# Performance work log

Hardware: AMD Instinct MI355X
Metric: run time of the kernel (lower is better)

## Reference

```python
import jax, jax.numpy as jnp
import numpy as np

N, E, IN_CH, EDGE_DIM, N_GRAPHS = 8000, 64000, 256, 16, 64
HEADS = (3, 2, 2, 1)
OUT_CH = (512, 512, 256, 256)
IN_CHS = (IN_CH, 1536, 1024, 512)
NEG_SLOPE = 0.2  # PyG GATv2Conv default negative_slope


def setup_inputs() -> dict:
    key = jax.random.key(0)
    ks = iter(jax.random.split(key, 64))
    d = {}
    d["x"] = jax.random.normal(next(ks), (N, IN_CH), jnp.float32)
    d["edge_index"] = jax.random.randint(next(ks), (2, E), 0, N, dtype=jnp.int32)
    d["edge_attr"] = jax.random.normal(next(ks), (E, EDGE_DIM), jnp.float32)
    d["batch"] = jnp.sort(jax.random.randint(next(ks), (N,), 0, N_GRAPHS, dtype=jnp.int32))
    for i, (ci, h, co) in enumerate(zip(IN_CHS, HEADS, OUT_CH), 1):
        hc = h * co
        s = 1.0 / np.sqrt(ci)
        d[f"W{i}l"] = (jax.random.normal(next(ks), (ci, hc)) * s).astype(jnp.float32)
        d[f"b{i}l"] = jnp.zeros((hc,), jnp.float32)
        d[f"W{i}r"] = (jax.random.normal(next(ks), (ci, hc)) * s).astype(jnp.float32)
        d[f"b{i}r"] = jnp.zeros((hc,), jnp.float32)
        d[f"W{i}e"] = (jax.random.normal(next(ks), (EDGE_DIM, hc)) / np.sqrt(EDGE_DIM)).astype(jnp.float32)
        d[f"att{i}"] = (jax.random.normal(next(ks), (h, co)) / np.sqrt(co)).astype(jnp.float32)
        d[f"bias{i}"] = jnp.zeros((hc,), jnp.float32)
    d["fc1_w"] = (jax.random.normal(next(ks), (256, 64)) / 16.0).astype(jnp.float32)
    d["fc1_b"] = jnp.zeros((64,), jnp.float32)
    d["fc2_w"] = (jax.random.normal(next(ks), (64, 1)) / 8.0).astype(jnp.float32)
    d["fc2_b"] = jnp.zeros((1,), jnp.float32)
    return d


def gatv2(x, src, dst, ea, Wl, bl, Wr, br, We, att, bias, heads, co):
    """GATv2Conv forward (PyG semantics, self-loops already appended in src/dst/ea)."""
    n = x.shape[0]
    xl = (x @ Wl + bl).reshape(n, heads, co)  # applied to source nodes
    xr = (x @ Wr + br).reshape(n, heads, co)  # applied to target nodes
    ee = (ea @ We).reshape(-1, heads, co)     # edge embedding (no bias in PyG)
    m = xl[src] + xr[dst] + ee                # [E', H, C]
    logits = jnp.einsum('ehc,hc->eh', jax.nn.leaky_relu(m, NEG_SLOPE), att)
    # segmented softmax over incoming edges per destination node
    lmax = jax.ops.segment_max(logits, dst, num_segments=n)
    p = jnp.exp(logits - lmax[dst])
    denom = jax.ops.segment_sum(p, dst, num_segments=n)
    alpha = p / denom[dst]                    # every node has a self-loop -> denom > 0
    out = jax.ops.segment_sum(alpha[:, :, None] * xl[src], dst, num_segments=n)
    return out.reshape(n, heads * co) + bias


def _forward(x, edge_index, edge_attr, batch, params, fc):
    n = x.shape[0]
    src0, dst0 = edge_index[0], edge_index[1]
    # add_self_loops with fill_value='mean': per-destination mean of incoming edge_attr
    ea_sum = jax.ops.segment_sum(edge_attr, dst0, num_segments=n)
    ea_cnt = jax.ops.segment_sum(jnp.ones((edge_attr.shape[0], 1), edge_attr.dtype), dst0, num_segments=n)
    ea_loop = ea_sum / jnp.maximum(ea_cnt, 1.0)
    loop = jnp.arange(n, dtype=edge_index.dtype)
    src = jnp.concatenate([src0, loop])
    dst = jnp.concatenate([dst0, loop])
    ea = jnp.concatenate([edge_attr, ea_loop])
    h = x
    for p, hds, co in zip(params, HEADS, OUT_CH):
        h = jax.nn.relu(gatv2(h, src, dst, ea, *p, hds, co))
    # global mean pool over graphs
    s = jax.ops.segment_sum(h, batch, num_segments=N_GRAPHS)
    cnt = jax.ops.segment_sum(jnp.ones((n, 1), h.dtype), batch, num_segments=N_GRAPHS)
    g = s / jnp.maximum(cnt, 1.0)
    # dropout is identity in eval mode
    fc1_w, fc1_b, fc2_w, fc2_b = fc
    g = jax.nn.relu(g @ fc1_w + fc1_b)
    return g @ fc2_w + fc2_b


def reference(x, edge_index, edge_attr, batch,
              W1l, b1l, W1r, b1r, W1e, att1, bias1,
              W2l, b2l, W2r, b2r, W2e, att2, bias2,
              W3l, b3l, W3r, b3r, W3e, att3, bias3,
              W4l, b4l, W4r, b4r, W4e, att4, bias4,
              fc1_w, fc1_b, fc2_w, fc2_b):
    params = [(W1l, b1l, W1r, b1r, W1e, att1, bias1),
              (W2l, b2l, W2r, b2r, W2e, att2, bias2),
              (W3l, b3l, W3r, b3r, W3e, att3, bias3),
              (W4l, b4l, W4r, b4r, W4e, att4, bias4)]
    return _forward(x, edge_index, edge_attr, batch, params, (fc1_w, fc1_b, fc2_w, fc2_b))
```

## Files before the change

### kernel.cpp

```cpp
#include <hip/hip_runtime.h>
#include <math.h>

#define N_NODES 8000
#define N_EDGES 64000
#define ETOT    (N_EDGES + N_NODES)
#define EDIM    16
#define NGRAPHS 64

typedef __attribute__((ext_vector_type(8))) short short8v;
typedef __attribute__((ext_vector_type(4))) short short4v;
typedef __attribute__((ext_vector_type(4))) float f32x4;

__device__ inline unsigned short f2bf(float f) {
    unsigned u = __builtin_bit_cast(unsigned, f);
    unsigned r = (u + 0x7FFF + ((u >> 16) & 1)) >> 16;
    return (unsigned short)r;
}
__device__ inline float bf2f(unsigned short b) {
    unsigned u = ((unsigned)b) << 16;
    return __builtin_bit_cast(float, u);
}

__device__ inline void gload16(const void* g, void* l) {
    __builtin_amdgcn_global_load_lds(
        (const __attribute__((address_space(1))) void*)g,
        (__attribute__((address_space(3))) void*)l, 16, 0, 0);
}


__global__ void count_deg(const int* __restrict__ dst0, int* __restrict__ deg) {
    int e = blockIdx.x * 256 + threadIdx.x;
    if (e < N_EDGES) atomicAdd(&deg[dst0[e]], 1);
}

__global__ void scan_deg2(const int* __restrict__ deg, int* __restrict__ rowptr,
                          int* __restrict__ woff) {
    __shared__ int stot[256];
    int t = threadIdx.x;
    int base = t * 32;
    int sum = 0;
    for (int j = 0; j < 32; j++) {
        int i = base + j;
        if (i < N_NODES) sum += deg[i] + 1;
    }
    stot[t] = sum;
    __syncthreads();
    for (int off = 1; off < 256; off <<= 1) {
        int u = (t >= off) ? stot[t - off] : 0;
        __syncthreads();
        stot[t] += u;
        __syncthreads();
    }
    int run = (t == 0) ? 0 : stot[t - 1];
    if (t == 0) rowptr[0] = 0;
    for (int j = 0; j < 32; j++) {
        int i = base + j;
        if (i < N_NODES) {
            int v = deg[i] + 1;
            woff[i] = run;
            rowptr[i + 1] = run + v;
            run += v;
        }
    }
}

__global__ void fill_eid(const int* __restrict__ dst0, int* __restrict__ woff,
                         int* __restrict__ eid) {
    int i = blockIdx.x * 256 + threadIdx.x;
    if (i < N_EDGES) {
        int pos = atomicAdd(&woff[dst0[i]], 1);
        eid[pos] = i;
    } else if (i < ETOT) {
        int n = i - N_EDGES;
        int pos = atomicAdd(&woff[n], 1);
        eid[pos] = i;
    }
}

__global__ void csr_fill_dst(const int* __restrict__ rowptr, int* __restrict__ csr_dst) {
    int n = blockIdx.x * 256 + threadIdx.x;
    if (n >= N_NODES) return;
    int b = rowptr[n], t = rowptr[n + 1];
    for (int i = b; i < t; i++) csr_dst[i] = n;
}

__global__ void ea_loop_kernel(const int* __restrict__ rowptr, const int* __restrict__ eid,
                               const float* __restrict__ edge_attr, float* __restrict__ ea_loop) {
    int n = blockIdx.x * 256 + threadIdx.x;
    if (n >= N_NODES) return;
    float s[EDIM];
#pragma unroll
    for (int k = 0; k < EDIM; k++) s[k] = 0.f;
    int cnt = 0;
    int b = rowptr[n], t = rowptr[n + 1];
    for (int i = b; i < t; i++) {
        int e = eid[i];
        if (e < N_EDGES) {
            cnt++;
            const float* ea = edge_attr + (size_t)e * EDIM;
#pragma unroll
            for (int k = 0; k < EDIM; k++) s[k] += ea[k];
        }
    }
    float inv = 1.f / (float)(cnt > 0 ? cnt : 1);
#pragma unroll
    for (int k = 0; k < EDIM; k++) ea_loop[(size_t)n * EDIM + k] = s[k] * inv;
}

__global__ void csr_srcea_bf(const int* __restrict__ eid, const int* __restrict__ src0,
                             const float* __restrict__ edge_attr, const float* __restrict__ ea_loop,
                             int* __restrict__ csr_src,
                             short* __restrict__ eah, short* __restrict__ eal) {
    int t = blockIdx.x * 256 + threadIdx.x;
    int i = t >> 2, q = t & 3;
    if (i >= ETOT) return;
    int e = eid[i];
    int s = (e < N_EDGES) ? src0[e] : (e - N_EDGES);
    if (q == 0) csr_src[i] = s;
    const float* ea = (e < N_EDGES) ? edge_attr + (size_t)e * EDIM
                                    : ea_loop + (size_t)(e - N_EDGES) * EDIM;
    float4 v = *(const float4*)(ea + q * 4);
    unsigned short h0 = f2bf(v.x), h1 = f2bf(v.y), h2 = f2bf(v.z), h3 = f2bf(v.w);
    short4v hv = { (short)h0, (short)h1, (short)h2, (short)h3 };
    short4v lv = { (short)f2bf(v.x - bf2f(h0)), (short)f2bf(v.y - bf2f(h1)),
                   (short)f2bf(v.z - bf2f(h2)), (short)f2bf(v.w - bf2f(h3)) };
    short4v zv = { 0, 0, 0, 0 };
    *(short4v*)(eah + (size_t)i * 32 + q * 4) = hv;
    *(short4v*)(eal + (size_t)i * 32 + q * 4) = lv;
    *(short4v*)(eah + (size_t)i * 32 + 16 + q * 4) = zv;
    *(short4v*)(eal + (size_t)i * 32 + 16 + q * 4) = zv;
}

__global__ void cvt_we_all(const float* __restrict__ We1, const float* __restrict__ We2,
                           const float* __restrict__ We3, const float* __restrict__ We4,
                           short* __restrict__ weTh, short* __restrict__ weTl) {
    int ch = blockIdx.x * 256 + threadIdx.x;
    if (ch >= 3328) return;
    const float* We; int lch, hc;
    if (ch < 1536)      { We = We1; lch = ch;        hc = 1536; }
    else if (ch < 2560) { We = We2; lch = ch - 1536; hc = 1024; }
    else if (ch < 3072) { We = We3; lch = ch - 2560; hc = 512;  }
    else                { We = We4; lch = ch - 3072; hc = 256;  }
#pragma unroll
    for (int k = 0; k < EDIM; k++) {
        float v = We[(size_t)k * hc + lch];
        unsigned short h = f2bf(v);
        unsigned short l = f2bf(v - bf2f(h));
        weTh[(size_t)ch * 32 + k] = (short)h;
        weTl[(size_t)ch * 32 + k] = (short)l;
    }
#pragma unroll
    for (int k = EDIM; k < 32; k++) {
        weTh[(size_t)ch * 32 + k] = 0;
        weTl[(size_t)ch * 32 + k] = 0;
    }
}


__global__ __launch_bounds__(256) void cvt_wt_t2(
        const float* __restrict__ Wl, const float* __restrict__ Wr,
        short* __restrict__ WTh, short* __restrict__ WTl, int K, int Nc) {
    __shared__ float sh[32][33];
    const float* W = blockIdx.z ? Wr : Wl;
    size_t obase = blockIdx.z ? (size_t)Nc * K : 0;
    int t = threadIdx.x;
    int tx = t & 31, ty = t >> 5;
    int n0 = blockIdx.x * 32, k0 = blockIdx.y * 32;
#pragma unroll
    for (int j = 0; j < 4; j++)
        sh[ty + j * 8][tx] = W[(size_t)(k0 + ty + j * 8) * Nc + n0 + tx];
    __syncthreads();
#pragma unroll
    for (int j = 0; j < 4; j++) {
        int row = ty + j * 8;
        float v = sh[tx][row];
        unsigned short h = f2bf(v);
        unsigned short l = f2bf(v - bf2f(h));
        size_t idx = obase + (size_t)(n0 + row) * K + k0 + tx;
        WTh[idx] = (short)h;
        WTl[idx] = (short)l;
    }
}


__global__ __launch_bounds__(256) void cvt_act(
        const float* __restrict__ in, short* __restrict__ acth, short* __restrict__ actl,
        int total ) {
    int i = blockIdx.x * 256 + threadIdx.x;
    if (i * 4 >= total) return;
    float4 v = *(const float4*)(in + (size_t)i * 4);
    unsigned short h0 = f2bf(v.x), h1 = f2bf(v.y), h2 = f2bf(v.z), h3 = f2bf(v.w);
    short4v hv = { (short)h0, (short)h1, (short)h2, (short)h3 };
    short4v lv = { (short)f2bf(v.x - bf2f(h0)), (short)f2bf(v.y - bf2f(h1)),
                   (short)f2bf(v.z - bf2f(h2)), (short)f2bf(v.w - bf2f(h3)) };
    *(short4v*)(acth + (size_t)i * 4) = hv;
    *(short4v*)(actl + (size_t)i * 4) = lv;
}


__global__ __launch_bounds__(256) void gemm_mfma5(
        const short* __restrict__ Ah_g, const short* __restrict__ Al_g,
        const short* __restrict__ BTh, const short* __restrict__ BTl,
        const float* __restrict__ bias1, const float* __restrict__ bias2, int hsplit,
        float* __restrict__ C, int M, int K, int Nc) {
    __shared__ __align__(16) short lds[4 * 128 * 32];
    int t = threadIdx.x;

    int gx = gridDim.x;
    int nwg = gx * gridDim.y;
    int orig = blockIdx.y * gx + blockIdx.x;
    int q = nwg >> 3, r = nwg & 7;
    int xcd = orig & 7, pos = orig >> 3;
    int nid = (xcd < r ? xcd * (q + 1) : r * (q + 1) + (xcd - r) * q) + pos;
    int bx = nid % gx, by = nid / gx;
    int m0 = by * 128, n0 = bx * 128;

    int lane = t & 63, wave = t >> 6;
    int wm = (wave >> 1) * 64, wn = (wave & 1) * 64;
    int fr = lane & 15, quad = lane >> 4;

    int rl = lane >> 2, seg = lane & 3;
    int perm = seg ^ ((rl >> 1) & 3);
    const short* gp = (wave == 0) ? Ah_g : (wave == 1) ? Al_g : (wave == 2) ? BTh : BTl;
    int brow = (wave < 2) ? m0 : n0;
    const short* src = gp + (size_t)(brow + rl) * K + perm * 8;
    short* ldsw = &lds[wave * 4096];

    int ks = (quad ^ ((fr >> 1) & 3)) << 3;

    f32x4 acc[4][4];
#pragma unroll
    for (int i = 0; i < 4; i++)
#pragma unroll
        for (int j = 0; j < 4; j++) acc[i][j] = (f32x4)(0.f);

    for (int k0 = 0; k0 < K; k0 += 32) {
        __syncthreads();
#pragma unroll
        for (int g = 0; g < 8; g++)
            gload16(src + k0 + (size_t)g * 16 * K, ldsw + g * 512);
        __syncthreads();

        short8v ah[4], al[4], bh[4], bl[4];
#pragma unroll
        for (int mi = 0; mi < 4; mi++) {
            int rr = (wm + mi * 16 + fr) * 32 + ks;
            ah[mi] = *(short8v*)&lds[rr];
            al[mi] = *(short8v*)&lds[4096 + rr];
        }
#pragma unroll
        for (int ni = 0; ni < 4; ni++) {
            int rr = (wn + ni * 16 + fr) * 32 + ks;
            bh[ni] = *(short8v*)&lds[8192 + rr];
            bl[ni] = *(short8v*)&lds[12288 + rr];
        }
#pragma unroll
        for (int mi = 0; mi < 4; mi++)
#pragma unroll
            for (int ni = 0; ni < 4; ni++) {
                acc[mi][ni] = __builtin_amdgcn_mfma_f32_16x16x32_bf16(
                    al[mi], bh[ni], acc[mi][ni], 0, 0, 0);
                acc[mi][ni] = __builtin_amdgcn_mfma_f32_16x16x32_bf16(
                    ah[mi], bl[ni], acc[mi][ni], 0, 0, 0);
                acc[mi][ni] = __builtin_amdgcn_mfma_f32_16x16x32_bf16(
                    ah[mi], bh[ni], acc[mi][ni], 0, 0, 0);
            }
    }

    int rbase = (lane >> 4) * 4;
#pragma unroll
    for (int ni = 0; ni < 4; ni++) {
        int col = n0 + wn + ni * 16 + fr;
        const float* bp = (col < hsplit) ? bias1 + col : bias2 + (col - hsplit);
        float bz = *bp;
#pragma unroll
        for (int mi = 0; mi < 4; mi++) {
            int row0 = m0 + wm + mi * 16 + rbase;
#pragma unroll
            for (int rr = 0; rr < 4; rr++) {
                int row = row0 + rr;
                if (row < M) C[(size_t)row * Nc + col] = acc[mi][ni][rr] + bz;
            }
        }
    }
}


__global__ __launch_bounds__(256, 4) void edge_logits7(
        const float* __restrict__ xl, const float* __restrict__ xr,
        const short* __restrict__ weTh, const short* __restrict__ weTl,
        const float* __restrict__ att,
        const short* __restrict__ eah, const short* __restrict__ eal,
        const int* __restrict__ csr_src, const int* __restrict__ csr_dst,
        float* __restrict__ logits, int H, int co, int stride) {
    int tid = threadIdx.x;
    int lane = tid & 63, wave = tid >> 6;
    int head = blockIdx.y;
    int cbase = head * co;
    int e0 = blockIdx.x * 64 + wave * 16;
    int col = lane & 15;
    int quad = lane >> 4;
    int e = e0 + col;
    int s = csr_src[e], d = csr_dst[e];
    int ch0 = cbase + quad * 4;

    short8v bh = *(const short8v*)(eah + (size_t)e * 32 + quad * 8);
    short8v bl = *(const short8v*)(eal + (size_t)e * 32 + quad * 8);

    const float* xls = xl + (size_t)s * stride + ch0;
    const float* xrd = xr + (size_t)d * stride + ch0;
    const float* atp = att + ch0;
    const short* wph = weTh + (size_t)(cbase + col) * 32 + quad * 8;
    const short* wpl = weTl + (size_t)(cbase + col) * 32 + quad * 8;

    int ntile = co >> 4;
    float p = 0.f;

    short8v ahA = *(const short8v*)wph;
    short8v alA = *(const short8v*)wpl;
    float4 lvA = *(const float4*)xls;
    float4 rvA = *(const float4*)xrd;
    float4 avA = *(const float4*)atp;

    for (int tt = 0; tt < ntile - 1; tt++) {
        short8v ahB = *(const short8v*)(wph + (size_t)(tt + 1) * 512);
        short8v alB = *(const short8v*)(wpl + (size_t)(tt + 1) * 512);
        float4 lvB = *(const float4*)(xls + (tt + 1) * 16);
        float4 rvB = *(const float4*)(xrd + (tt + 1) * 16);
        float4 avB = *(const float4*)(atp + (tt + 1) * 16);

        f32x4 ee = (f32x4)(0.f);
        ee = __builtin_amdgcn_mfma_f32_16x16x32_bf16(ahA, bl, ee, 0, 0, 0);
        ee = __builtin_amdgcn_mfma_f32_16x16x32_bf16(alA, bh, ee, 0, 0, 0);
        ee = __builtin_amdgcn_mfma_f32_16x16x32_bf16(ahA, bh, ee, 0, 0, 0);
        float m0 = lvA.x + rvA.x + ee[0];
        float m1 = lvA.y + rvA.y + ee[1];
        float m2 = lvA.z + rvA.z + ee[2];
        float m3 = lvA.w + rvA.w + ee[3];
        m0 = (m0 > 0.f) ? m0 : 0.2f * m0;
        m1 = (m1 > 0.f) ? m1 : 0.2f * m1;
        m2 = (m2 > 0.f) ? m2 : 0.2f * m2;
        m3 = (m3 > 0.f) ? m3 : 0.2f * m3;
        p += m0 * avA.x + m1 * avA.y + m2 * avA.z + m3 * avA.w;

        ahA = ahB; alA = alB; lvA = lvB; rvA = rvB; avA = avB;
    }
    {
        f32x4 ee = (f32x4)(0.f);
        ee = __builtin_amdgcn_mfma_f32_16x16x32_bf16(ahA, bl, ee, 0, 0, 0);
        ee = __builtin_amdgcn_mfma_f32_16x16x32_bf16(alA, bh, ee, 0, 0, 0);
        ee = __builtin_amdgcn_mfma_f32_16x16x32_bf16(ahA, bh, ee, 0, 0, 0);
        float m0 = lvA.x + rvA.x + ee[0];
        float m1 = lvA.y + rvA.y + ee[1];
        float m2 = lvA.z + rvA.z + ee[2];
        float m3 = lvA.w + rvA.w + ee[3];
        m0 = (m0 > 0.f) ? m0 : 0.2f * m0;
        m1 = (m1 > 0.f) ? m1 : 0.2f * m1;
        m2 = (m2 > 0.f) ? m2 : 0.2f * m2;
        m3 = (m3 > 0.f) ? m3 : 0.2f * m3;
        p += m0 * avA.x + m1 * avA.y + m2 * avA.z + m3 * avA.w;
    }

    p += __shfl_down(p, 32, 64);
    p += __shfl_down(p, 16, 64);
    if (lane < 16)
        logits[(size_t)(e0 + lane) * H + head] = p;
}


__global__ __launch_bounds__(256) void aggregate5(
        const int* __restrict__ rowptr, const int* __restrict__ csr_src,
        const float* __restrict__ logits, const float* __restrict__ xl,
        const float* __restrict__ bias,
        short* __restrict__ outh, short* __restrict__ outl,
        float* __restrict__ outf, int last,
        int H, int co_shift, int hc, int stride) {
    __shared__ int ssrc[64];
    __shared__ float salp[64][4];
    __shared__ float sm[4], sinv[4];
    int n = blockIdx.x;
    int b = rowptr[n], t = rowptr[n + 1];
    int tid = threadIdx.x;
    int nthr = blockDim.x;

    if (tid < H) {
        float m = -1e30f;
        for (int i = b; i < t; i++)
            m = fmaxf(m, logits[(size_t)i * H + tid]);
        float s = 0.f;
        for (int i = b; i < t; i++)
            s += expf(logits[(size_t)i * H + tid] - m);
        sm[tid] = m;
        sinv[tid] = 1.f / s;
    }
    __syncthreads();

    int j0 = tid * 4;
    int j1 = j0 + nthr * 4;
    int h0 = j0 >> co_shift;
    int h1 = j1 >> co_shift;
    bool act1 = j1 < hc;

    float4 acc0 = make_float4(0.f, 0.f, 0.f, 0.f);
    float4 acc1 = make_float4(0.f, 0.f, 0.f, 0.f);

    for (int cb = b; cb < t; cb += 64) {
        int m = min(64, t - cb);
        __syncthreads();
        for (int i = tid; i < m; i += nthr) {
            ssrc[i] = csr_src[cb + i];
            for (int h = 0; h < H; h++)
                salp[i][h] = expf(logits[(size_t)(cb + i) * H + h] - sm[h]) * sinv[h];
        }
        __syncthreads();
        for (int i = 0; i < m; i++) {
            int s = ssrc[i];
            const float* base = xl + (size_t)s * stride;
            {
                float a = salp[i][h0];
                float4 v = *(const float4*)(base + j0);
                acc0.x += a * v.x; acc0.y += a * v.y;
                acc0.z += a * v.z; acc0.w += a * v.w;
            }
            if (act1) {
                float a = salp[i][h1];
                float4 v = *(const float4*)(base + j1);
                acc1.x += a * v.x; acc1.y += a * v.y;
                acc1.z += a * v.z; acc1.w += a * v.w;
            }
        }
    }

    float4 bz0 = *(const float4*)(bias + j0);
    float4 o0;
    o0.x = fmaxf(acc0.x + bz0.x, 0.f); o0.y = fmaxf(acc0.y + bz0.y, 0.f);
    o0.z = fmaxf(acc0.z + bz0.z, 0.f); o0.w = fmaxf(acc0.w + bz0.w, 0.f);
    if (last) {
        *(float4*)(outf + (size_t)n * hc + j0) = o0;
    } else {
        unsigned short hx = f2bf(o0.x), hy = f2bf(o0.y), hz = f2bf(o0.z), hw = f2bf(o0.w);
        short4v hv = { (short)hx, (short)hy, (short)hz, (short)hw };
        short4v lv = { (short)f2bf(o0.x - bf2f(hx)), (short)f2bf(o0.y - bf2f(hy)),
                       (short)f2bf(o0.z - bf2f(hz)), (short)f2bf(o0.w - bf2f(hw)) };
        *(short4v*)(outh + (size_t)n * hc + j0) = hv;
        *(short4v*)(outl + (size_t)n * hc + j0) = lv;
    }
    if (act1) {
        float4 bz1 = *(const float4*)(bias + j1);
        float4 o1;
        o1.x = fmaxf(acc1.x + bz1.x, 0.f); o1.y = fmaxf(acc1.y + bz1.y, 0.f);
        o1.z = fmaxf(acc1.z + bz1.z, 0.f); o1.w = fmaxf(acc1.w + bz1.w, 0.f);
        if (last) {
            *(float4*)(outf + (size_t)n * hc + j1) = o1;
        } else {
            unsigned short hx = f2bf(o1.x), hy = f2bf(o1.y), hz = f2bf(o1.z), hw = f2bf(o1.w);
            short4v hv = { (short)hx, (short)hy, (short)hz, (short)hw };
            short4v lv = { (short)f2bf(o1.x - bf2f(hx)), (short)f2bf(o1.y - bf2f(hy)),
                           (short)f2bf(o1.z - bf2f(hz)), (short)f2bf(o1.w - bf2f(hw)) };
            *(short4v*)(outh + (size_t)n * hc + j1) = hv;
            *(short4v*)(outl + (size_t)n * hc + j1) = lv;
        }
    }
}


__global__ void pool_cnt(const int* __restrict__ batch, int* __restrict__ gcnt) {
    int n = blockIdx.x * 256 + threadIdx.x;
    if (n < N_NODES) atomicAdd(&gcnt[batch[n]], 1);
}

__global__ void graph_scan(const int* __restrict__ gcnt, int* __restrict__ gstart) {
    if (threadIdx.x == 0) {
        int run = 0;
        for (int g = 0; g < NGRAPHS; g++) { gstart[g] = run; run += gcnt[g]; }
        gstart[NGRAPHS] = run;
    }
}

__global__ void pool_sum2(const int* __restrict__ gstart, const float* __restrict__ h,
                          float* __restrict__ pooled) {
    int g = blockIdx.x, qtr = blockIdx.y;
    int b = gstart[g], e = gstart[g + 1];
    int cnt = e - b;
    int lo = b + (cnt * qtr) / 4, hi = b + (cnt * (qtr + 1)) / 4;
    if (lo >= hi) return;
    int c = threadIdx.x;
    float s = 0.f;
    for (int n = lo; n < hi; n++) s += h[(size_t)n * 256 + c];
    atomicAdd(&pooled[g * 256 + c], s);
}

__global__ void mlp_head(const float* __restrict__ pooled, const int* __restrict__ gcnt,
                         const float* __restrict__ fc1w, const float* __restrict__ fc1b,
                         const float* __restrict__ fc2w, const float* __restrict__ fc2b,
                         float* __restrict__ out) {
    int g = threadIdx.x;
    if (g >= NGRAPHS) return;
    float inv = 1.f / (float)(gcnt[g] > 0 ? gcnt[g] : 1);
    float s[64];
#pragma unroll
    for (int j = 0; j < 64; j++) s[j] = fc1b[j];
    for (int c = 0; c < 256; c++) {
        float mv = pooled[g * 256 + c] * inv;
#pragma unroll
        for (int j = 0; j < 64; j++) s[j] += mv * fc1w[c * 64 + j];
    }
    float o = 0.f;
#pragma unroll
    for (int j = 0; j < 64; j++) o += fmaxf(s[j], 0.f) * fc2w[j];
    out[g] = o + fc2b[0];
}


extern "C" void kernel_launch(void* const* d_in, const int* in_sizes, int n_in,
                              void* d_out, int out_size, void* d_ws, size_t ws_size,
                              hipStream_t stream) {
    const float* x         = (const float*)d_in[0];
    const int*   edge_index= (const int*)d_in[1];
    const float* edge_attr = (const float*)d_in[2];
    const int*   batch     = (const int*)d_in[3];
    const int* src0 = edge_index;
    const int* dst0 = edge_index + N_EDGES;

    const float *Wl[4], *bl[4], *Wr[4], *br[4], *We[4], *att[4], *bias[4];
    for (int i = 0; i < 4; i++) {
        int base = 4 + 7 * i;
        Wl[i]   = (const float*)d_in[base + 0];
        bl[i]   = (const float*)d_in[base + 1];
        Wr[i]   = (const float*)d_in[base + 2];
        br[i]   = (const float*)d_in[base + 3];
        We[i]   = (const float*)d_in[base + 4];
        att[i]  = (const float*)d_in[base + 5];
        bias[i] = (const float*)d_in[base + 6];
    }
    const float* fc1w = (const float*)d_in[32];
    const float* fc1b = (const float*)d_in[33];
    const float* fc2w = (const float*)d_in[34];
    const float* fc2b = (const float*)d_in[35];
    float* out = (float*)d_out;

    float* ws = (float*)d_ws;
    int*   rowptr  = (int*)(ws + 0);
    int*   woff    = (int*)(ws + 8064);
    int*   eid     = (int*)(ws + 16128);
    int*   csr_src = (int*)(ws + 88128);
    int*   csr_dst = (int*)(ws + 160128);
    float* ea_loop = ws + 232128;
    short* weTh_a  = (short*)(ws + 360128);
    short* weTl_a  = (short*)(ws + 413376);
    int*   gstart  = (int*)(ws + 470000);
    float* logits  = ws + 1512128;
    float* xlr     = ws + 1728128;
    float* hbF     = xlr + 24576000;
    float* pooled  = hbF + 12288000;
    int*   gcnt    = (int*)(pooled + 16384);
    short* wth     = (short*)(ws + 38608640);
    short* wtl     = (short*)(ws + 40181504);
    short* eah     = (short*)(ws + 41754368);
    short* eal     = (short*)(ws + 42906368);
    short* acth    = (short*)(ws + 44107520);
    short* actl    = (short*)(ws + 50300672);

    hipMemsetAsync(woff, 0, N_NODES * sizeof(int), stream);
    count_deg<<<(N_EDGES + 255) / 256, 256, 0, stream>>>(dst0, woff);
    scan_deg2<<<1, 256, 0, stream>>>(woff, rowptr, woff);
    fill_eid<<<(ETOT + 255) / 256, 256, 0, stream>>>(dst0, woff, eid);
    csr_fill_dst<<<(N_NODES + 255) / 256, 256, 0, stream>>>(rowptr, csr_dst);
    ea_loop_kernel<<<(N_NODES + 255) / 256, 256, 0, stream>>>(rowptr, eid, edge_attr, ea_loop);
    csr_srcea_bf<<<(ETOT * 4 + 255) / 256, 256, 0, stream>>>(eid, src0, edge_attr, ea_loop,
                                                             csr_src, eah, eal);
    cvt_we_all<<<(3328 + 255) / 256, 256, 0, stream>>>(We[0], We[1], We[2], We[3],
                                                       weTh_a, weTl_a);
    cvt_act<<<(N_NODES * 256 / 4 + 255) / 256, 256, 0, stream>>>(x, acth, actl, N_NODES * 256);

    const int IN[4] = {256, 1536, 1024, 512};
    const int HH[4] = {3, 2, 2, 1};
    const int CO[4] = {512, 512, 256, 256};
    const int CS[4] = {9, 9, 8, 8};
    const int CHOFF[4] = {0, 1536, 2560, 3072};

    for (int L = 0; L < 4; L++) {
        int K = IN[L], H = HH[L], co = CO[L], hc = H * co, cs = CS[L];
        int hc2 = 2 * hc;
        dim3 gg(hc2 / 128, (N_NODES + 127) / 128);
        dim3 gw(hc / 32, K / 32, 2);
        cvt_wt_t2<<<gw, 256, 0, stream>>>(Wl[L], Wr[L], wth, wtl, K, hc);
        gemm_mfma5<<<gg, 256, 0, stream>>>(acth, actl, wth, wtl,
                                           bl[L], br[L], hc, xlr, N_NODES, K, hc2);
        dim3 gl(ETOT / 64, H);
        edge_logits7<<<gl, 256, 0, stream>>>(
            xlr, xlr + hc,
            weTh_a + (size_t)CHOFF[L] * 32, weTl_a + (size_t)CHOFF[L] * 32,
            att[L], eah, eal, csr_src, csr_dst, logits, H, co, hc2);
        int athr = hc / 4 > 256 ? 256 : hc / 4;
        aggregate5<<<N_NODES, athr, 0, stream>>>(
            rowptr, csr_src, logits, xlr, bias[L],
            acth, actl, hbF, (L == 3) ? 1 : 0, H, cs, hc, hc2);
    }

    hipMemsetAsync(pooled, 0, (16384 + 64) * sizeof(float), stream);
    pool_cnt<<<(N_NODES + 255) / 256, 256, 0, stream>>>(batch, gcnt);
    graph_scan<<<1, 64, 0, stream>>>(gcnt, gstart);
    dim3 gp(NGRAPHS, 4);
    pool_sum2<<<gp, 256, 0, stream>>>(gstart, hbF, pooled);
    mlp_head<<<1, 64, 0, stream>>>(pooled, gcnt, fc1w, fc1b, fc2w, fc2b, out);
}
```

Baseline: 1.150 ms.

## Fuse edge logits and aggregation into one online-softmax kernel per node

Replaces the separate edge_logits MFMA kernel and the aggregate kernel with a single per-destination-node kernel. It computes each incoming edge's logit with FP32 FMAs against register-held edge weights, then applies an online softmax with running max and denominator while accumulating gathered source features. This drops the logits buffer round-trip, the csr_dst and bf16 hi/lo edge-attr preprocessing, and one launch per layer. In exchange, every edge now needs a block-wide reduction and two __syncthreads, tid 0 does the serial softmax update, and blocks grow to up to 384 threads carrying large per-thread weight registers.

Measured after the change: 1.669 ms. 1.45x slower.

```diff
diff --git a/kernel.cpp b/kernel.cpp
--- a/kernel.cpp
+++ b/kernel.cpp
@@ -77,13 +77,6 @@
     }
 }
 
-__global__ void csr_fill_dst(const int* __restrict__ rowptr, int* __restrict__ csr_dst) {
-    int n = blockIdx.x * 256 + threadIdx.x;
-    if (n >= N_NODES) return;
-    int b = rowptr[n], t = rowptr[n + 1];
-    for (int i = b; i < t; i++) csr_dst[i] = n;
-}
-
 __global__ void ea_loop_kernel(const int* __restrict__ rowptr, const int* __restrict__ eid,
                                const float* __restrict__ edge_attr, float* __restrict__ ea_loop) {
     int n = blockIdx.x * 256 + threadIdx.x;
@@ -107,10 +100,9 @@
     for (int k = 0; k < EDIM; k++) ea_loop[(size_t)n * EDIM + k] = s[k] * inv;
 }
 
-__global__ void csr_srcea_bf(const int* __restrict__ eid, const int* __restrict__ src0,
-                             const float* __restrict__ edge_attr, const float* __restrict__ ea_loop,
-                             int* __restrict__ csr_src,
-                             short* __restrict__ eah, short* __restrict__ eal) {
+__global__ void csr_src_ea(const int* __restrict__ eid, const int* __restrict__ src0,
+                           const float* __restrict__ edge_attr, const float* __restrict__ ea_loop,
+                           int* __restrict__ csr_src, float* __restrict__ ea_csr) {
     int t = blockIdx.x * 256 + threadIdx.x;
     int i = t >> 2, q = t & 3;
     if (i >= ETOT) return;
@@ -119,21 +111,12 @@
     if (q == 0) csr_src[i] = s;
     const float* ea = (e < N_EDGES) ? edge_attr + (size_t)e * EDIM
                                     : ea_loop + (size_t)(e - N_EDGES) * EDIM;
-    float4 v = *(const float4*)(ea + q * 4);
-    unsigned short h0 = f2bf(v.x), h1 = f2bf(v.y), h2 = f2bf(v.z), h3 = f2bf(v.w);
-    short4v hv = { (short)h0, (short)h1, (short)h2, (short)h3 };
-    short4v lv = { (short)f2bf(v.x - bf2f(h0)), (short)f2bf(v.y - bf2f(h1)),
-                   (short)f2bf(v.z - bf2f(h2)), (short)f2bf(v.w - bf2f(h3)) };
-    short4v zv = { 0, 0, 0, 0 };
-    *(short4v*)(eah + (size_t)i * 32 + q * 4) = hv;
-    *(short4v*)(eal + (size_t)i * 32 + q * 4) = lv;
-    *(short4v*)(eah + (size_t)i * 32 + 16 + q * 4) = zv;
-    *(short4v*)(eal + (size_t)i * 32 + 16 + q * 4) = zv;
-}
-
-__global__ void cvt_we_all(const float* __restrict__ We1, const float* __restrict__ We2,
-                           const float* __restrict__ We3, const float* __restrict__ We4,
-                           short* __restrict__ weTh, short* __restrict__ weTl) {
+    *(float4*)(ea_csr + (size_t)i * 16 + q * 4) = *(const float4*)(ea + q * 4);
+}
+
+__global__ void cvt_weT(const float* __restrict__ We1, const float* __restrict__ We2,
+                        const float* __restrict__ We3, const float* __restrict__ We4,
+                        float* __restrict__ weT) {
     int ch = blockIdx.x * 256 + threadIdx.x;
     if (ch >= 3328) return;
     const float* We; int lch, hc;
@@ -142,18 +125,8 @@
     else if (ch < 3072) { We = We3; lch = ch - 2560; hc = 512;  }
     else                { We = We4; lch = ch - 3072; hc = 256;  }
 #pragma unroll
-    for (int k = 0; k < EDIM; k++) {
-        float v = We[(size_t)k * hc + lch];
-        unsigned short h = f2bf(v);
-        unsigned short l = f2bf(v - bf2f(h));
-        weTh[(size_t)ch * 32 + k] = (short)h;
-        weTl[(size_t)ch * 32 + k] = (short)l;
-    }
-#pragma unroll
-    for (int k = EDIM; k < 32; k++) {
-        weTh[(size_t)ch * 32 + k] = 0;
-        weTl[(size_t)ch * 32 + k] = 0;
-    }
+    for (int k = 0; k < EDIM; k++)
+        weT[(size_t)ch * 16 + k] = We[(size_t)k * hc + lch];
 }
 
 
@@ -286,180 +259,126 @@
 }
 
 
-__global__ __launch_bounds__(256, 4) void edge_logits7(
-        const float* __restrict__ xl, const float* __restrict__ xr,
-        const short* __restrict__ weTh, const short* __restrict__ weTl,
-        const float* __restrict__ att,
-        const short* __restrict__ eah, const short* __restrict__ eal,
-        const int* __restrict__ csr_src, const int* __restrict__ csr_dst,
-        float* __restrict__ logits, int H, int co, int stride) {
-    int tid = threadIdx.x;
-    int lane = tid & 63, wave = tid >> 6;
-    int head = blockIdx.y;
-    int cbase = head * co;
-    int e0 = blockIdx.x * 64 + wave * 16;
-    int col = lane & 15;
-    int quad = lane >> 4;
-    int e = e0 + col;
-    int s = csr_src[e], d = csr_dst[e];
-    int ch0 = cbase + quad * 4;
-
-    short8v bh = *(const short8v*)(eah + (size_t)e * 32 + quad * 8);
-    short8v bl = *(const short8v*)(eal + (size_t)e * 32 + quad * 8);
-
-    const float* xls = xl + (size_t)s * stride + ch0;
-    const float* xrd = xr + (size_t)d * stride + ch0;
-    const float* atp = att + ch0;
-    const short* wph = weTh + (size_t)(cbase + col) * 32 + quad * 8;
-    const short* wpl = weTl + (size_t)(cbase + col) * 32 + quad * 8;
-
-    int ntile = co >> 4;
-    float p = 0.f;
-
-    short8v ahA = *(const short8v*)wph;
-    short8v alA = *(const short8v*)wpl;
-    float4 lvA = *(const float4*)xls;
-    float4 rvA = *(const float4*)xrd;
-    float4 avA = *(const float4*)atp;
-
-    for (int tt = 0; tt < ntile - 1; tt++) {
-        short8v ahB = *(const short8v*)(wph + (size_t)(tt + 1) * 512);
-        short8v alB = *(const short8v*)(wpl + (size_t)(tt + 1) * 512);
-        float4 lvB = *(const float4*)(xls + (tt + 1) * 16);
-        float4 rvB = *(const float4*)(xrd + (tt + 1) * 16);
-        float4 avB = *(const float4*)(atp + (tt + 1) * 16);
-
-        f32x4 ee = (f32x4)(0.f);
-        ee = __builtin_amdgcn_mfma_f32_16x16x32_bf16(ahA, bl, ee, 0, 0, 0);
-        ee = __builtin_amdgcn_mfma_f32_16x16x32_bf16(alA, bh, ee, 0, 0, 0);
-        ee = __builtin_amdgcn_mfma_f32_16x16x32_bf16(ahA, bh, ee, 0, 0, 0);
-        float m0 = lvA.x + rvA.x + ee[0];
-        float m1 = lvA.y + rvA.y + ee[1];
-        float m2 = lvA.z + rvA.z + ee[2];
-        float m3 = lvA.w + rvA.w + ee[3];
-        m0 = (m0 > 0.f) ? m0 : 0.2f * m0;
-        m1 = (m1 > 0.f) ? m1 : 0.2f * m1;
-        m2 = (m2 > 0.f) ? m2 : 0.2f * m2;
-        m3 = (m3 > 0.f) ? m3 : 0.2f * m3;
-        p += m0 * avA.x + m1 * avA.y + m2 * avA.z + m3 * avA.w;
-
-        ahA = ahB; alA = alB; lvA = lvB; rvA = rvB; avA = avB;
-    }
-    {
-        f32x4 ee = (f32x4)(0.f);
-        ee = __builtin_amdgcn_mfma_f32_16x16x32_bf16(ahA, bl, ee, 0, 0, 0);
-        ee = __builtin_amdgcn_mfma_f32_16x16x32_bf16(alA, bh, ee, 0, 0, 0);
-        ee = __builtin_amdgcn_mfma_f32_16x16x32_bf16(ahA, bh, ee, 0, 0, 0);
-        float m0 = lvA.x + rvA.x + ee[0];
-        float m1 = lvA.y + rvA.y + ee[1];
-        float m2 = lvA.z + rvA.z + ee[2];
-        float m3 = lvA.w + rvA.w + ee[3];
-        m0 = (m0 > 0.f) ? m0 : 0.2f * m0;
-        m1 = (m1 > 0.f) ? m1 : 0.2f * m1;
-        m2 = (m2 > 0.f) ? m2 : 0.2f * m2;
-        m3 = (m3 > 0.f) ? m3 : 0.2f * m3;
-        p += m0 * avA.x + m1 * avA.y + m2 * avA.z + m3 * avA.w;
-    }
-
-    p += __shfl_down(p, 32, 64);
-    p += __shfl_down(p, 16, 64);
-    if (lane < 16)
-        logits[(size_t)(e0 + lane) * H + head] = p;
-}
-
-
-__global__ __launch_bounds__(256) void aggregate5(
+__global__ __launch_bounds__(384) void edge_agg(
         const int* __restrict__ rowptr, const int* __restrict__ csr_src,
-        const float* __restrict__ logits, const float* __restrict__ xl,
+        const float* __restrict__ ea_csr, const float* __restrict__ weT,
+        const float* __restrict__ att, const float* __restrict__ xlr,
         const float* __restrict__ bias,
         short* __restrict__ outh, short* __restrict__ outl,
         float* __restrict__ outf, int last,
         int H, int co_shift, int hc, int stride) {
-    __shared__ int ssrc[64];
-    __shared__ float salp[64][4];
-    __shared__ float sm[4], sinv[4];
+    __shared__ __align__(16) float sea[2][16];
+    __shared__ float sbin[8];
+    __shared__ float sm[4], sd[4], sf[4], sw[4];
     int n = blockIdx.x;
     int b = rowptr[n], t = rowptr[n + 1];
+    int deg = t - b;
     int tid = threadIdx.x;
-    int nthr = blockDim.x;
-
-    if (tid < H) {
-        float m = -1e30f;
-        for (int i = b; i < t; i++)
-            m = fmaxf(m, logits[(size_t)i * H + tid]);
-        float s = 0.f;
-        for (int i = b; i < t; i++)
-            s += expf(logits[(size_t)i * H + tid] - m);
-        sm[tid] = m;
-        sinv[tid] = 1.f / s;
+    int lane = tid & 63, wid = tid >> 6;
+    int j0 = tid * 4;
+    int h0 = j0 >> co_shift;
+    int nw = (int)blockDim.x >> 6;
+    int wph = nw / H;
+
+    const float* xl = xlr;
+    const float* xr = xlr + hc;
+
+    f32x4 xrv = *(const f32x4*)(xr + (size_t)n * stride + j0);
+    f32x4 at4 = *(const f32x4*)(att + j0);
+    f32x4 wreg[4][4];
+#pragma unroll
+    for (int rr = 0; rr < 4; rr++)
+#pragma unroll
+        for (int kq = 0; kq < 4; kq++)
+            wreg[rr][kq] = *(const f32x4*)(weT + (size_t)(j0 + rr) * 16 + kq * 4);
+
+    if (tid < 4) {
+        sm[tid] = -1e30f; sd[tid] = 0.f;
+        *(f32x4*)&sea[0][tid * 4] = *(const f32x4*)(ea_csr + (size_t)b * 16 + tid * 4);
     }
     __syncthreads();
 
-    int j0 = tid * 4;
-    int j1 = j0 + nthr * 4;
-    int h0 = j0 >> co_shift;
-    int h1 = j1 >> co_shift;
-    bool act1 = j1 < hc;
-
-    float4 acc0 = make_float4(0.f, 0.f, 0.f, 0.f);
-    float4 acc1 = make_float4(0.f, 0.f, 0.f, 0.f);
-
-    for (int cb = b; cb < t; cb += 64) {
-        int m = min(64, t - cb);
+    int s_cur = csr_src[b];
+    f32x4 xlv = *(const f32x4*)(xl + (size_t)s_cur * stride + j0);
+    f32x4 acc = (f32x4)(0.f);
+
+    for (int i = 0; i < deg; i++) {
+        f32x4 xln = xlv;
+        if (i + 1 < deg) {
+            int s_nx = csr_src[b + i + 1];
+            xln = *(const f32x4*)(xl + (size_t)s_nx * stride + j0);
+            if (tid < 4)
+                *(f32x4*)&sea[(i + 1) & 1][tid * 4] =
+                    *(const f32x4*)(ea_csr + (size_t)(b + i + 1) * 16 + tid * 4);
+        }
+
+        const float* se = sea[i & 1];
+        f32x4 e0 = *(const f32x4*)(se);
+        f32x4 e1 = *(const f32x4*)(se + 4);
+        f32x4 e2 = *(const f32x4*)(se + 8);
+        f32x4 e3 = *(const f32x4*)(se + 12);
+        float pd = 0.f;
+#pragma unroll
+        for (int rr = 0; rr < 4; rr++) {
+            float ee =
+                e0[0]*wreg[rr][0][0] + e0[1]*wreg[rr][0][1] + e0[2]*wreg[rr][0][2] + e0[3]*wreg[rr][0][3] +
+                e1[0]*wreg[rr][1][0] + e1[1]*wreg[rr][1][1] + e1[2]*wreg[rr][1][2] + e1[3]*wreg[rr][1][3] +
+                e2[0]*wreg[rr][2][0] + e2[1]*wreg[rr][2][1] + e2[2]*wreg[rr][2][2] + e2[3]*wreg[rr][2][3] +
+                e3[0]*wreg[rr][3][0] + e3[1]*wreg[rr][3][1] + e3[2]*wreg[rr][3][2] + e3[3]*wreg[rr][3][3];
+            float m = xlv[rr] + xrv[rr] + ee;
+            float lr = (m > 0.f) ? m : 0.2f * m;
+            pd += at4[rr] * lr;
+        }
+
+        pd += __shfl_down(pd, 32, 64);
+        pd += __shfl_down(pd, 16, 64);
+        pd += __shfl_down(pd, 8, 64);
+        pd += __shfl_down(pd, 4, 64);
+        pd += __shfl_down(pd, 2, 64);
+        pd += __shfl_down(pd, 1, 64);
+        if (lane == 0) sbin[wid] = pd;
         __syncthreads();
-        for (int i = tid; i < m; i += nthr) {
-            ssrc[i] = csr_src[cb + i];
-            for (int h = 0; h < H; h++)
-                salp[i][h] = expf(logits[(size_t)(cb + i) * H + h] - sm[h]) * sinv[h];
+
+        if (tid == 0) {
+#pragma unroll
+            for (int h = 0; h < 3; h++) {
+                if (h >= H) break;
+                float L = 0.f;
+                for (int w = h * wph; w < (h + 1) * wph; w++) L += sbin[w];
+                float mo = sm[h];
+                float mx = fmaxf(mo, L);
+                float f = expf(mo - mx);
+                float wg = expf(L - mx);
+                sd[h] = sd[h] * f + wg;
+                sm[h] = mx;
+                sf[h] = f; sw[h] = wg;
+            }
         }
         __syncthreads();
-        for (int i = 0; i < m; i++) {
-            int s = ssrc[i];
-            const float* base = xl + (size_t)s * stride;
-            {
-                float a = salp[i][h0];
-                float4 v = *(const float4*)(base + j0);
-                acc0.x += a * v.x; acc0.y += a * v.y;
-                acc0.z += a * v.z; acc0.w += a * v.w;
-            }
-            if (act1) {
-                float a = salp[i][h1];
-                float4 v = *(const float4*)(base + j1);
-                acc1.x += a * v.x; acc1.y += a * v.y;
-                acc1.z += a * v.z; acc1.w += a * v.w;
-            }
-        }
-    }
-
-    float4 bz0 = *(const float4*)(bias + j0);
-    float4 o0;
-    o0.x = fmaxf(acc0.x + bz0.x, 0.f); o0.y = fmaxf(acc0.y + bz0.y, 0.f);
-    o0.z = fmaxf(acc0.z + bz0.z, 0.f); o0.w = fmaxf(acc0.w + bz0.w, 0.f);
+
+        float f = sf[h0], wg = sw[h0];
+#pragma unroll
+        for (int rr = 0; rr < 4; rr++)
+            acc[rr] = acc[rr] * f + wg * xlv[rr];
+        xlv = xln;
+    }
+
+    float inv = 1.f / sd[h0];
+    f32x4 bz = *(const f32x4*)(bias + j0);
+    f32x4 o;
+#pragma unroll
+    for (int rr = 0; rr < 4; rr++)
+        o[rr] = fmaxf(acc[rr] * inv + bz[rr], 0.f);
+
     if (last) {
-        *(float4*)(outf + (size_t)n * hc + j0) = o0;
+        *(f32x4*)(outf + (size_t)n * hc + j0) = o;
     } else {
-        unsigned short hx = f2bf(o0.x), hy = f2bf(o0.y), hz = f2bf(o0.z), hw = f2bf(o0.w);
+        unsigned short hx = f2bf(o[0]), hy = f2bf(o[1]), hz = f2bf(o[2]), hw = f2bf(o[3]);
         short4v hv = { (short)hx, (short)hy, (short)hz, (short)hw };
-        short4v lv = { (short)f2bf(o0.x - bf2f(hx)), (short)f2bf(o0.y - bf2f(hy)),
-                       (short)f2bf(o0.z - bf2f(hz)), (short)f2bf(o0.w - bf2f(hw)) };
+        short4v lv = { (short)f2bf(o[0] - bf2f(hx)), (short)f2bf(o[1] - bf2f(hy)),
+                       (short)f2bf(o[2] - bf2f(hz)), (short)f2bf(o[3] - bf2f(hw)) };
         *(short4v*)(outh + (size_t)n * hc + j0) = hv;
         *(short4v*)(outl + (size_t)n * hc + j0) = lv;
-    }
-    if (act1) {
-        float4 bz1 = *(const float4*)(bias + j1);
-        float4 o1;
-        o1.x = fmaxf(acc1.x + bz1.x, 0.f); o1.y = fmaxf(acc1.y + bz1.y, 0.f);
-        o1.z = fmaxf(acc1.z + bz1.z, 0.f); o1.w = fmaxf(acc1.w + bz1.w, 0.f);
-        if (last) {
-            *(float4*)(outf + (size_t)n * hc + j1) = o1;
-        } else {
-            unsigned short hx = f2bf(o1.x), hy = f2bf(o1.y), hz = f2bf(o1.z), hw = f2bf(o1.w);
-            short4v hv = { (short)hx, (short)hy, (short)hz, (short)hw };
-            short4v lv = { (short)f2bf(o1.x - bf2f(hx)), (short)f2bf(o1.y - bf2f(hy)),
-                           (short)f2bf(o1.z - bf2f(hz)), (short)f2bf(o1.w - bf2f(hw)) };
-            *(short4v*)(outh + (size_t)n * hc + j1) = hv;
-            *(short4v*)(outl + (size_t)n * hc + j1) = lv;
-        }
     }
 }
 
@@ -544,20 +463,16 @@
     int*   woff    = (int*)(ws + 8064);
     int*   eid     = (int*)(ws + 16128);
     int*   csr_src = (int*)(ws + 88128);
-    int*   csr_dst = (int*)(ws + 160128);
     float* ea_loop = ws + 232128;
-    short* weTh_a  = (short*)(ws + 360128);
-    short* weTl_a  = (short*)(ws + 413376);
-    int*   gstart  = (int*)(ws + 470000);
-    float* logits  = ws + 1512128;
+    float* weT     = ws + 360128;
+    float* ea_csr  = ws + 470000;
+    int*   gstart  = (int*)(ws + 1700000);
     float* xlr     = ws + 1728128;
     float* hbF     = xlr + 24576000;
     float* pooled  = hbF + 12288000;
     int*   gcnt    = (int*)(pooled + 16384);
     short* wth     = (short*)(ws + 38608640);
     short* wtl     = (short*)(ws + 40181504);
-    short* eah     = (short*)(ws + 41754368);
-    short* eal     = (short*)(ws + 42906368);
     short* acth    = (short*)(ws + 44107520);
     short* actl    = (short*)(ws + 50300672);
 
@@ -565,12 +480,10 @@
     count_deg<<<(N_EDGES + 255) / 256, 256, 0, stream>>>(dst0, woff);
     scan_deg2<<<1, 256, 0, stream>>>(woff, rowptr, woff);
     fill_eid<<<(ETOT + 255) / 256, 256, 0, stream>>>(dst0, woff, eid);
-    csr_fill_dst<<<(N_NODES + 255) / 256, 256, 0, stream>>>(rowptr, csr_dst);
     ea_loop_kernel<<<(N_NODES + 255) / 256, 256, 0, stream>>>(rowptr, eid, edge_attr, ea_loop);
-    csr_srcea_bf<<<(ETOT * 4 + 255) / 256, 256, 0, stream>>>(eid, src0, edge_attr, ea_loop,
-                                                             csr_src, eah, eal);
-    cvt_we_all<<<(3328 + 255) / 256, 256, 0, stream>>>(We[0], We[1], We[2], We[3],
-                                                       weTh_a, weTl_a);
+    csr_src_ea<<<(ETOT * 4 + 255) / 256, 256, 0, stream>>>(eid, src0, edge_attr, ea_loop,
+                                                           csr_src, ea_csr);
+    cvt_weT<<<(3328 + 255) / 256, 256, 0, stream>>>(We[0], We[1], We[2], We[3], weT);
     cvt_act<<<(N_NODES * 256 / 4 + 255) / 256, 256, 0, stream>>>(x, acth, actl, N_NODES * 256);
 
     const int IN[4] = {256, 1536, 1024, 512};
@@ -587,14 +500,10 @@
         cvt_wt_t2<<<gw, 256, 0, stream>>>(Wl[L], Wr[L], wth, wtl, K, hc);
         gemm_mfma5<<<gg, 256, 0, stream>>>(acth, actl, wth, wtl,
                                            bl[L], br[L], hc, xlr, N_NODES, K, hc2);
-        dim3 gl(ETOT / 64, H);
-        edge_logits7<<<gl, 256, 0, stream>>>(
-            xlr, xlr + hc,
-            weTh_a + (size_t)CHOFF[L] * 32, weTl_a + (size_t)CHOFF[L] * 32,
-            att[L], eah, eal, csr_src, csr_dst, logits, H, co, hc2);
-        int athr = hc / 4 > 256 ? 256 : hc / 4;
-        aggregate5<<<N_NODES, athr, 0, stream>>>(
-            rowptr, csr_src, logits, xlr, bias[L],
+        int athr = hc / 4;
+        edge_agg<<<N_NODES, athr, 0, stream>>>(
+            rowptr, csr_src, ea_csr, weT + (size_t)CHOFF[L] * 16,
+            att[L], xlr, bias[L],
             acth, actl, hbF, (L == 3) ? 1 : 0, H, cs, hc, hc2);
     }
 
```

## Replace MFMA split-bf16 edge embedding with fp32 FMA and atomic logit reduction

Applied to the files above, without the earlier changes.

Rewrites the edge-logit kernel so that each lane owns four channels, keeps its slice of the edge-weight matrix in registers and computes the edge embedding with plain fp32 FMAs. This replaces the three bf16 MFMAs per tile used for split-precision emulation. Work is split over 256-channel slices, with a full-wave shuffle reduction per edge and an atomicAdd into logits, which is now zeroed by a memset in every layer. Edge attributes and We stay in fp32, so the bf16 hi/lo conversion kernels go away. The cost is a 6-step shuffle plus one atomic per edge per slice, and many more scalar FMAs.

Result: slower. 1.251 ms (+8.8%).

```diff
diff --git a/kernel.cpp b/kernel.cpp
--- a/kernel.cpp
+++ b/kernel.cpp
@@ -107,10 +107,9 @@
     for (int k = 0; k < EDIM; k++) ea_loop[(size_t)n * EDIM + k] = s[k] * inv;
 }
 
-__global__ void csr_srcea_bf(const int* __restrict__ eid, const int* __restrict__ src0,
-                             const float* __restrict__ edge_attr, const float* __restrict__ ea_loop,
-                             int* __restrict__ csr_src,
-                             short* __restrict__ eah, short* __restrict__ eal) {
+__global__ void csr_src_ea(const int* __restrict__ eid, const int* __restrict__ src0,
+                           const float* __restrict__ edge_attr, const float* __restrict__ ea_loop,
+                           int* __restrict__ csr_src, float* __restrict__ ea_csr) {
     int t = blockIdx.x * 256 + threadIdx.x;
     int i = t >> 2, q = t & 3;
     if (i >= ETOT) return;
@@ -119,21 +118,12 @@
     if (q == 0) csr_src[i] = s;
     const float* ea = (e < N_EDGES) ? edge_attr + (size_t)e * EDIM
                                     : ea_loop + (size_t)(e - N_EDGES) * EDIM;
-    float4 v = *(const float4*)(ea + q * 4);
-    unsigned short h0 = f2bf(v.x), h1 = f2bf(v.y), h2 = f2bf(v.z), h3 = f2bf(v.w);
-    short4v hv = { (short)h0, (short)h1, (short)h2, (short)h3 };
-    short4v lv = { (short)f2bf(v.x - bf2f(h0)), (short)f2bf(v.y - bf2f(h1)),
-                   (short)f2bf(v.z - bf2f(h2)), (short)f2bf(v.w - bf2f(h3)) };
-    short4v zv = { 0, 0, 0, 0 };
-    *(short4v*)(eah + (size_t)i * 32 + q * 4) = hv;
-    *(short4v*)(eal + (size_t)i * 32 + q * 4) = lv;
-    *(short4v*)(eah + (size_t)i * 32 + 16 + q * 4) = zv;
-    *(short4v*)(eal + (size_t)i * 32 + 16 + q * 4) = zv;
-}
-
-__global__ void cvt_we_all(const float* __restrict__ We1, const float* __restrict__ We2,
-                           const float* __restrict__ We3, const float* __restrict__ We4,
-                           short* __restrict__ weTh, short* __restrict__ weTl) {
+    *(float4*)(ea_csr + (size_t)i * 16 + q * 4) = *(const float4*)(ea + q * 4);
+}
+
+__global__ void cvt_weT(const float* __restrict__ We1, const float* __restrict__ We2,
+                        const float* __restrict__ We3, const float* __restrict__ We4,
+                        float* __restrict__ weT) {
     int ch = blockIdx.x * 256 + threadIdx.x;
     if (ch >= 3328) return;
     const float* We; int lch, hc;
@@ -142,18 +132,8 @@
     else if (ch < 3072) { We = We3; lch = ch - 2560; hc = 512;  }
     else                { We = We4; lch = ch - 3072; hc = 256;  }
 #pragma unroll
-    for (int k = 0; k < EDIM; k++) {
-        float v = We[(size_t)k * hc + lch];
-        unsigned short h = f2bf(v);
-        unsigned short l = f2bf(v - bf2f(h));
-        weTh[(size_t)ch * 32 + k] = (short)h;
-        weTl[(size_t)ch * 32 + k] = (short)l;
-    }
-#pragma unroll
-    for (int k = EDIM; k < 32; k++) {
-        weTh[(size_t)ch * 32 + k] = 0;
-        weTl[(size_t)ch * 32 + k] = 0;
-    }
+    for (int k = 0; k < EDIM; k++)
+        weT[(size_t)ch * 16 + k] = We[(size_t)k * hc + lch];
 }
 
 
@@ -286,85 +266,61 @@
 }
 
 
-__global__ __launch_bounds__(256, 4) void edge_logits7(
-        const float* __restrict__ xl, const float* __restrict__ xr,
-        const short* __restrict__ weTh, const short* __restrict__ weTl,
-        const float* __restrict__ att,
-        const short* __restrict__ eah, const short* __restrict__ eal,
+__global__ __launch_bounds__(256) void edge_logits8(
         const int* __restrict__ csr_src, const int* __restrict__ csr_dst,
-        float* __restrict__ logits, int H, int co, int stride) {
+        const float* __restrict__ ea_csr, const float* __restrict__ weT,
+        const float* __restrict__ att, const float* __restrict__ xlr,
+        float* __restrict__ logits, int H, int co_shift, int hc, int stride) {
     int tid = threadIdx.x;
     int lane = tid & 63, wave = tid >> 6;
-    int head = blockIdx.y;
-    int cbase = head * co;
+    int sl = blockIdx.y;
+    int head = (sl << 8) >> co_shift;
+    int cb = (sl << 8) + lane * 4;
     int e0 = blockIdx.x * 64 + wave * 16;
-    int col = lane & 15;
-    int quad = lane >> 4;
-    int e = e0 + col;
-    int s = csr_src[e], d = csr_dst[e];
-    int ch0 = cbase + quad * 4;
-
-    short8v bh = *(const short8v*)(eah + (size_t)e * 32 + quad * 8);
-    short8v bl = *(const short8v*)(eal + (size_t)e * 32 + quad * 8);
-
-    const float* xls = xl + (size_t)s * stride + ch0;
-    const float* xrd = xr + (size_t)d * stride + ch0;
-    const float* atp = att + ch0;
-    const short* wph = weTh + (size_t)(cbase + col) * 32 + quad * 8;
-    const short* wpl = weTl + (size_t)(cbase + col) * 32 + quad * 8;
-
-    int ntile = co >> 4;
-    float p = 0.f;
-
-    short8v ahA = *(const short8v*)wph;
-    short8v alA = *(const short8v*)wpl;
-    float4 lvA = *(const float4*)xls;
-    float4 rvA = *(const float4*)xrd;
-    float4 avA = *(const float4*)atp;
-
-    for (int tt = 0; tt < ntile - 1; tt++) {
-        short8v ahB = *(const short8v*)(wph + (size_t)(tt + 1) * 512);
-        short8v alB = *(const short8v*)(wpl + (size_t)(tt + 1) * 512);
-        float4 lvB = *(const float4*)(xls + (tt + 1) * 16);
-        float4 rvB = *(const float4*)(xrd + (tt + 1) * 16);
-        float4 avB = *(const float4*)(atp + (tt + 1) * 16);
-
-        f32x4 ee = (f32x4)(0.f);
-        ee = __builtin_amdgcn_mfma_f32_16x16x32_bf16(ahA, bl, ee, 0, 0, 0);
-        ee = __builtin_amdgcn_mfma_f32_16x16x32_bf16(alA, bh, ee, 0, 0, 0);
-        ee = __builtin_amdgcn_mfma_f32_16x16x32_bf16(ahA, bh, ee, 0, 0, 0);
-        float m0 = lvA.x + rvA.x + ee[0];
-        float m1 = lvA.y + rvA.y + ee[1];
-        float m2 = lvA.z + rvA.z + ee[2];
-        float m3 = lvA.w + rvA.w + ee[3];
-        m0 = (m0 > 0.f) ? m0 : 0.2f * m0;
-        m1 = (m1 > 0.f) ? m1 : 0.2f * m1;
-        m2 = (m2 > 0.f) ? m2 : 0.2f * m2;
-        m3 = (m3 > 0.f) ? m3 : 0.2f * m3;
-        p += m0 * avA.x + m1 * avA.y + m2 * avA.z + m3 * avA.w;
-
-        ahA = ahB; alA = alB; lvA = lvB; rvA = rvB; avA = avB;
-    }
-    {
-        f32x4 ee = (f32x4)(0.f);
-        ee = __builtin_amdgcn_mfma_f32_16x16x32_bf16(ahA, bl, ee, 0, 0, 0);
-        ee = __builtin_amdgcn_mfma_f32_16x16x32_bf16(alA, bh, ee, 0, 0, 0);
-        ee = __builtin_amdgcn_mfma_f32_16x16x32_bf16(ahA, bh, ee, 0, 0, 0);
-        float m0 = lvA.x + rvA.x + ee[0];
-        float m1 = lvA.y + rvA.y + ee[1];
-        float m2 = lvA.z + rvA.z + ee[2];
-        float m3 = lvA.w + rvA.w + ee[3];
-        m0 = (m0 > 0.f) ? m0 : 0.2f * m0;
-        m1 = (m1 > 0.f) ? m1 : 0.2f * m1;
-        m2 = (m2 > 0.f) ? m2 : 0.2f * m2;
-        m3 = (m3 > 0.f) ? m3 : 0.2f * m3;
-        p += m0 * avA.x + m1 * avA.y + m2 * avA.z + m3 * avA.w;
-    }
-
-    p += __shfl_down(p, 32, 64);
-    p += __shfl_down(p, 16, 64);
-    if (lane < 16)
-        logits[(size_t)(e0 + lane) * H + head] = p;
+
+    const float* xl = xlr;
+    const float* xr = xlr + hc;
+
+    f32x4 at4 = *(const f32x4*)(att + cb);
+    f32x4 wreg[4][4];
+#pragma unroll
+    for (int rr = 0; rr < 4; rr++)
+#pragma unroll
+        for (int kq = 0; kq < 4; kq++)
+            wreg[rr][kq] = *(const f32x4*)(weT + (size_t)(cb + rr) * 16 + kq * 4);
+
+#pragma unroll 4
+    for (int c = 0; c < 16; c++) {
+        int e = e0 + c;
+        int s = csr_src[e], d = csr_dst[e];
+        const float* ea = ea_csr + (size_t)e * 16;
+        f32x4 e0v = *(const f32x4*)(ea);
+        f32x4 e1v = *(const f32x4*)(ea + 4);
+        f32x4 e2v = *(const f32x4*)(ea + 8);
+        f32x4 e3v = *(const f32x4*)(ea + 12);
+        f32x4 xlv = *(const f32x4*)(xl + (size_t)s * stride + cb);
+        f32x4 xrv = *(const f32x4*)(xr + (size_t)d * stride + cb);
+        float p = 0.f;
+#pragma unroll
+        for (int rr = 0; rr < 4; rr++) {
+            float ee =
+                e0v[0]*wreg[rr][0][0] + e0v[1]*wreg[rr][0][1] + e0v[2]*wreg[rr][0][2] + e0v[3]*wreg[rr][0][3] +
+                e1v[0]*wreg[rr][1][0] + e1v[1]*wreg[rr][1][1] + e1v[2]*wreg[rr][1][2] + e1v[3]*wreg[rr][1][3] +
+                e2v[0]*wreg[rr][2][0] + e2v[1]*wreg[rr][2][1] + e2v[2]*wreg[rr][2][2] + e2v[3]*wreg[rr][2][3] +
+                e3v[0]*wreg[rr][3][0] + e3v[1]*wreg[rr][3][1] + e3v[2]*wreg[rr][3][2] + e3v[3]*wreg[rr][3][3];
+            float m = xlv[rr] + xrv[rr] + ee;
+            float lr = (m > 0.f) ? m : 0.2f * m;
+            p += at4[rr] * lr;
+        }
+        p += __shfl_down(p, 32, 64);
+        p += __shfl_down(p, 16, 64);
+        p += __shfl_down(p, 8, 64);
+        p += __shfl_down(p, 4, 64);
+        p += __shfl_down(p, 2, 64);
+        p += __shfl_down(p, 1, 64);
+        if (lane == 0)
+            atomicAdd(&logits[(size_t)e * H + head], p);
+    }
 }
 
 
@@ -546,18 +502,16 @@
     int*   csr_src = (int*)(ws + 88128);
     int*   csr_dst = (int*)(ws + 160128);
     float* ea_loop = ws + 232128;
-    short* weTh_a  = (short*)(ws + 360128);
-    short* weTl_a  = (short*)(ws + 413376);
-    int*   gstart  = (int*)(ws + 470000);
-    float* logits  = ws + 1512128;
+    float* weT     = ws + 360128;
+    float* ea_csr  = ws + 470000;
+    int*   gstart  = (int*)(ws + 1700000);
     float* xlr     = ws + 1728128;
     float* hbF     = xlr + 24576000;
     float* pooled  = hbF + 12288000;
     int*   gcnt    = (int*)(pooled + 16384);
     short* wth     = (short*)(ws + 38608640);
     short* wtl     = (short*)(ws + 40181504);
-    short* eah     = (short*)(ws + 41754368);
-    short* eal     = (short*)(ws + 42906368);
+    float* logits  = ws + 41754368;
     short* acth    = (short*)(ws + 44107520);
     short* actl    = (short*)(ws + 50300672);
 
@@ -567,10 +521,9 @@
     fill_eid<<<(ETOT + 255) / 256, 256, 0, stream>>>(dst0, woff, eid);
     csr_fill_dst<<<(N_NODES + 255) / 256, 256, 0, stream>>>(rowptr, csr_dst);
     ea_loop_kernel<<<(N_NODES + 255) / 256, 256, 0, stream>>>(rowptr, eid, edge_attr, ea_loop);
-    csr_srcea_bf<<<(ETOT * 4 + 255) / 256, 256, 0, stream>>>(eid, src0, edge_attr, ea_loop,
-                                                             csr_src, eah, eal);
-    cvt_we_all<<<(3328 + 255) / 256, 256, 0, stream>>>(We[0], We[1], We[2], We[3],
-                                                       weTh_a, weTl_a);
+    csr_src_ea<<<(ETOT * 4 + 255) / 256, 256, 0, stream>>>(eid, src0, edge_attr, ea_loop,
+                                                           csr_src, ea_csr);
+    cvt_weT<<<(3328 + 255) / 256, 256, 0, stream>>>(We[0], We[1], We[2], We[3], weT);
     cvt_act<<<(N_NODES * 256 / 4 + 255) / 256, 256, 0, stream>>>(x, acth, actl, N_NODES * 256);
 
     const int IN[4] = {256, 1536, 1024, 512};
@@ -587,11 +540,11 @@
         cvt_wt_t2<<<gw, 256, 0, stream>>>(Wl[L], Wr[L], wth, wtl, K, hc);
         gemm_mfma5<<<gg, 256, 0, stream>>>(acth, actl, wth, wtl,
                                            bl[L], br[L], hc, xlr, N_NODES, K, hc2);
-        dim3 gl(ETOT / 64, H);
-        edge_logits7<<<gl, 256, 0, stream>>>(
-            xlr, xlr + hc,
-            weTh_a + (size_t)CHOFF[L] * 32, weTl_a + (size_t)CHOFF[L] * 32,
-            att[L], eah, eal, csr_src, csr_dst, logits, H, co, hc2);
+        hipMemsetAsync(logits, 0, (size_t)ETOT * H * sizeof(float), stream);
+        dim3 gl(ETOT / 64, hc >> 8);
+        edge_logits8<<<gl, 256, 0, stream>>>(
+            csr_src, csr_dst, ea_csr, weT + (size_t)CHOFF[L] * 16,
+            att[L], xlr, logits, H, cs, hc, hc2);
         int athr = hc / 4 > 256 ? 256 : hc / 4;
         aggregate5<<<N_NODES, athr, 0, stream>>>(
             rowptr, csr_src, logits, xlr, bias[L],
```
